# Kernel tuning notes

Measured on AMD Instinct MI355X. Metric: run time of the kernel, lower is better.

Reference implementation:

```python
import jax, jax.numpy as jnp
import numpy as np

N = 100000   # nodes
E = 600000   # edges
K = 3        # TAGConv hops
EPS = 1e-5   # BatchNorm eps
SLOPE = 0.01 # LeakyReLU negative slope


def setup_inputs() -> dict:
    key = jax.random.key(0)
    ks = jax.random.split(key, 8)
    y = jax.random.normal(ks[0], (N, 128), dtype=jnp.float32)
    edge_index = jax.random.randint(ks[1], (2, E), 0, N, dtype=jnp.int64)
    edge_attr = jax.random.uniform(ks[2], (E,), dtype=jnp.float32)
    # TAGConv layer l has (K+1) weight matrices [in, out]; bias only on first two layers
    W1 = 0.1 * jax.random.normal(ks[3], (K + 1, 128, 128), dtype=jnp.float32)
    b1 = jnp.full((128,), 0.1, dtype=jnp.float32)
    W2 = 0.1 * jax.random.normal(ks[4], (K + 1, 128, 128), dtype=jnp.float32)
    b2 = jnp.full((128,), 0.1, dtype=jnp.float32)
    W3 = 0.1 * jax.random.normal(ks[5], (K + 1, 128, 64), dtype=jnp.float32)
    g1 = jnp.ones((128,), jnp.float32); be1 = jnp.zeros((128,), jnp.float32)
    g2 = jnp.ones((128,), jnp.float32); be2 = jnp.zeros((128,), jnp.float32)
    g3 = jnp.ones((64,), jnp.float32);  be3 = jnp.zeros((64,), jnp.float32)
    return dict(y=y, edge_index=edge_index, edge_attr=edge_attr,
                W1=W1, b1=b1, g1=g1, be1=be1,
                W2=W2, b2=b2, g2=g2, be2=be2,
                W3=W3, g3=g3, be3=be3)


def _tag_conv(x, W, b, src, dst, norm):
    # out = sum_{k=0..K} A_hat^k x @ W_k (+ b)
    out = x @ W[0]
    h = x
    for k in range(1, W.shape[0]):
        h = jax.ops.segment_sum(norm[:, None] * h[src], dst, num_segments=N)
        out = out + h @ W[k]
    return out if b is None else out + b


def _bn(x, g, b):
    # BatchNorm1d training mode: biased batch stats over nodes
    m = x.mean(axis=0)
    v = jnp.mean((x - m) ** 2, axis=0)
    return (x - m) * jax.lax.rsqrt(v + EPS) * g + b


def reference(y, edge_index, edge_attr, W1, b1, g1, be1, W2, b2, g2, be2, W3, g3, be3):
    src, dst = edge_index[0], edge_index[1]
    # gcn_norm (symmetric, no self-loops): D^{-1/2} A D^{-1/2}
    deg = jax.ops.segment_sum(edge_attr, dst, num_segments=N)
    dis = jnp.where(deg > 0, jax.lax.rsqrt(jnp.maximum(deg, 1e-12)), 0.0)
    norm = dis[src] * edge_attr * dis[dst]
    lrelu = lambda t: jax.nn.leaky_relu(t, SLOPE)
    x = lrelu(_bn(_tag_conv(y, W1, b1, src, dst, norm), g1, be1))
    x = lrelu(_bn(_tag_conv(x, W2, b2, src, dst, norm), g2, be2))
    x = lrelu(_bn(_tag_conv(x, W3, None, src, dst, norm), g3, be3))
    return x
```

## Files before the change

### kernel.cpp

```cpp
#include <hip/hip_runtime.h>
#include <hip/hip_bf16.h>

typedef unsigned short b16;
typedef __attribute__((ext_vector_type(8))) unsigned short us8;
typedef __attribute__((ext_vector_type(8))) short short8;
typedef __attribute__((ext_vector_type(4))) float float4v;

#define NN 100000
#define NE 600000

__device__ __forceinline__ float bf2f(b16 u) {
    return __uint_as_float(((unsigned)u) << 16);
}
__device__ __forceinline__ b16 f2bf(float f) {
    unsigned x = __float_as_uint(f);
    return (b16)((x + 0x7fffu + ((x >> 16) & 1u)) >> 16);
}

__global__ void k_detect(const void* __restrict__ y, const void* __restrict__ ei,
                         int* __restrict__ flags) {
    if (threadIdx.x == 0 && blockIdx.x == 0) {
        const b16* p = (const b16*)y;
        int f32 = 0;
        for (int i = 0; i < 128; ++i) {
            float v = bf2f(p[i]);
            if (!(fabsf(v) < 1e4f)) { f32 = 1; break; }
        }
        flags[0] = f32;
        const long long* q = (const long long*)ei;
        int i64 = 1;
        for (int i = 0; i < 4; ++i) {
            long long v = q[i];
            if (v < 0 || v >= NN) i64 = 0;
        }
        flags[1] = i64;
    }
}

__global__ void k_cvt(const void* __restrict__ in, float* __restrict__ out, int n,
                      const int* __restrict__ flags) {
    int i = blockIdx.x * blockDim.x + threadIdx.x;
    if (i >= n) return;
    out[i] = flags[0] ? ((const float*)in)[i] : bf2f(((const b16*)in)[i]);
}

__global__ void k_idx(const void* __restrict__ ei, int* __restrict__ src32,
                      int* __restrict__ dst32, const int* __restrict__ flags) {
    int e = blockIdx.x * blockDim.x + threadIdx.x;
    if (e >= NE) return;
    int s, d;
    if (flags[1]) {
        const long long* p = (const long long*)ei;
        s = (int)p[e];
        d = (int)p[NE + e];
    } else {
        const int* p = (const int*)ei;
        s = p[e];
        d = p[NE + e];
    }
    src32[e] = ((unsigned)s < NN) ? s : 0;
    dst32[e] = ((unsigned)d < NN) ? d : 0;
}

__global__ void k_degcnt(const int* __restrict__ dst, const void* __restrict__ ea,
                         float* __restrict__ deg, int* __restrict__ cnt,
                         const int* __restrict__ flags) {
    int e = blockIdx.x * blockDim.x + threadIdx.x;
    if (e >= NE) return;
    float w = flags[0] ? ((const float*)ea)[e] : bf2f(((const b16*)ea)[e]);
    int d = dst[e];
    unsafeAtomicAdd(&deg[d], w);
    atomicAdd(&cnt[d], 1);
}

__global__ void k_dis(float* deg) {
    int n = blockIdx.x * blockDim.x + threadIdx.x;
    if (n < NN) {
        float d = deg[n];
        deg[n] = (d > 0.f) ? rsqrtf(fmaxf(d, 1e-12f)) : 0.f;
    }
}

#define SCAN_B 1024
#define SCAN_NB ((NN + SCAN_B - 1) / SCAN_B)

__global__ __launch_bounds__(SCAN_B) void k_scan1(const int* __restrict__ cnt,
                                                  int* __restrict__ inc,
                                                  int* __restrict__ bsum) {
    __shared__ int s[SCAN_B];
    int i = blockIdx.x * SCAN_B + threadIdx.x;
    s[threadIdx.x] = (i < NN) ? cnt[i] : 0;
    __syncthreads();
    for (int off = 1; off < SCAN_B; off <<= 1) {
        int t = (threadIdx.x >= off) ? s[threadIdx.x - off] : 0;
        __syncthreads();
        s[threadIdx.x] += t;
        __syncthreads();
    }
    if (i < NN) inc[i] = s[threadIdx.x];
    if (threadIdx.x == SCAN_B - 1) bsum[blockIdx.x] = s[SCAN_B - 1];
}

__global__ void k_scan2(int* bsum) {
    if (threadIdx.x == 0 && blockIdx.x == 0) {
        int a = 0;
        for (int i = 0; i < SCAN_NB; ++i) {
            int t = bsum[i];
            bsum[i] = a;
            a += t;
        }
    }
}

__global__ void k_scan3(const int* __restrict__ inc, const int* __restrict__ bsum,
                        int* __restrict__ rowptr) {
    int i = blockIdx.x * blockDim.x + threadIdx.x;
    if (i == 0) rowptr[0] = 0;
    if (i < NN) rowptr[i + 1] = inc[i] + bsum[i / SCAN_B];
}

__global__ void k_fill(const int* __restrict__ src, const int* __restrict__ dst,
                       const void* __restrict__ ea, const float* __restrict__ dis,
                       const int* __restrict__ rowptr, int* __restrict__ fill,
                       int* __restrict__ csrc, float* __restrict__ cw,
                       const int* __restrict__ flags) {
    int e = blockIdx.x * blockDim.x + threadIdx.x;
    if (e >= NE) return;
    float a = flags[0] ? ((const float*)ea)[e] : bf2f(((const b16*)ea)[e]);
    int d = dst[e];
    int s = src[e];
    int pos = rowptr[d] + atomicAdd(&fill[d], 1);
    csrc[pos] = s;
    cw[pos] = dis[s] * a * dis[d];
}

__global__ void k_pack(const void* __restrict__ W, b16* __restrict__ Wp, int NC,
                       const int* __restrict__ flags) {
    int f = blockIdx.x * blockDim.x + threadIdx.x;
    int total = 512 * NC / 8;
    if (f >= total) return;
    int lane = f & 63;
    int rest = f >> 6;
    int CT = NC >> 4;
    int ct = rest % CT, ks = rest / CT;
    int k0 = 32 * ks + (lane >> 4) * 8;
    int col = 16 * ct + (lane & 15);
    us8 v;
#pragma unroll
    for (int j = 0; j < 8; ++j) {
        float x = flags[0] ? ((const float*)W)[(size_t)(k0 + j) * NC + col]
                           : bf2f(((const b16*)W)[(size_t)(k0 + j) * NC + col]);
        v[j] = f2bf(x);
    }
    *(us8*)&Wp[(size_t)f * 8] = v;
}

__global__ void k_cast(const void* __restrict__ y, b16* __restrict__ XC,
                       const int* __restrict__ flags) {
    int i = blockIdx.x * blockDim.x + threadIdx.x;
    if (i >= NN * 32) return;
    int row = i >> 5, cg = i & 31;
    float4 v;
    if (flags[0]) {
        v = ((const float4*)y)[i];
    } else {
        ushort4 u = ((const ushort4*)y)[i];
        v = make_float4(bf2f(u.x), bf2f(u.y), bf2f(u.z), bf2f(u.w));
    }
    ushort4 o;
    o.x = f2bf(v.x); o.y = f2bf(v.y); o.z = f2bf(v.z); o.w = f2bf(v.w);
    *(ushort4*)&XC[(size_t)row * 512 + 4 * cg] = o;
}

__global__ __launch_bounds__(256) void k_spmm(b16* __restrict__ XC, int ci, int co,
                                              const int* __restrict__ rowptr,
                                              const int* __restrict__ csrc,
                                              const float* __restrict__ cw) {
    int gid = blockIdx.x * blockDim.x + threadIdx.x;
    int node = gid >> 6;
    if (node >= NN) return;
    int lane = gid & 63;
    int beg = rowptr[node], end = rowptr[node + 1];
    int coff = ci + 2 * lane;

    float ax0 = 0.f, ay0 = 0.f, ax1 = 0.f, ay1 = 0.f;
    for (int i = beg; i < end; i += 4) {
        int lim = end - 1;
        int e1 = i + 1, e2 = i + 2, e3 = i + 3;
        float w0 = cw[i];
        float w1 = (e1 < end) ? cw[e1] : 0.f;
        float w2 = (e2 < end) ? cw[e2] : 0.f;
        float w3 = (e3 < end) ? cw[e3] : 0.f;
        int s0 = csrc[i];
        int s1 = csrc[e1 < lim ? e1 : lim];
        int s2 = csrc[e2 < lim ? e2 : lim];
        int s3 = csrc[e3 < lim ? e3 : lim];
        unsigned u0 = *(const unsigned*)&XC[(size_t)s0 * 512 + coff];
        unsigned u1 = *(const unsigned*)&XC[(size_t)s1 * 512 + coff];
        unsigned u2 = *(const unsigned*)&XC[(size_t)s2 * 512 + coff];
        unsigned u3 = *(const unsigned*)&XC[(size_t)s3 * 512 + coff];
        ax0 = fmaf(w0, __uint_as_float(u0 << 16), ax0);
        ay0 = fmaf(w0, __uint_as_float(u0 & 0xFFFF0000u), ay0);
        ax1 = fmaf(w1, __uint_as_float(u1 << 16), ax1);
        ay1 = fmaf(w1, __uint_as_float(u1 & 0xFFFF0000u), ay1);
        ax0 = fmaf(w2, __uint_as_float(u2 << 16), ax0);
        ay0 = fmaf(w2, __uint_as_float(u2 & 0xFFFF0000u), ay0);
        ax1 = fmaf(w3, __uint_as_float(u3 << 16), ax1);
        ay1 = fmaf(w3, __uint_as_float(u3 & 0xFFFF0000u), ay1);
    }
    ax0 += ax1;
    ay0 += ay1;
    ushort2 o;
    o.x = f2bf(ax0);
    o.y = f2bf(ay0);
    *(ushort2*)&XC[(size_t)node * 512 + co + 2 * lane] = o;
}

template <int CTF>
__global__ __launch_bounds__(256) void k_mgemm(const b16* __restrict__ XC,
                                               const b16* __restrict__ Wp,
                                               const float* __restrict__ bias,
                                               b16* __restrict__ OUT,
                                               float* __restrict__ gsum,
                                               float* __restrict__ gsq) {
    constexpr int NC = CTF * 16;
    __shared__ float csum[64], csq[64];
    const int tid = threadIdx.x;
    const int wave = tid >> 6;
    const int lane = tid & 63;
    const int quad = lane >> 4;
    const int l15 = lane & 15;
    const int cb = blockIdx.y;
    const int cbase = cb * 4;
    const int rbase = blockIdx.x * 256 + wave * 64;

    for (int i = tid; i < 64; i += 256) {
        csum[i] = 0.f;
        csq[i] = 0.f;
    }

    float4v acc[4][4];
#pragma unroll
    for (int rt = 0; rt < 4; ++rt)
#pragma unroll
        for (int ct = 0; ct < 4; ++ct) acc[rt][ct] = (float4v)(0.f);

    const b16* gA[4];
#pragma unroll
    for (int rt = 0; rt < 4; ++rt) {
        int r = rbase + 16 * rt + l15;
        if (r >= NN) r = NN - 1;
        gA[rt] = XC + (size_t)r * 512 + quad * 8;
    }
    const b16* gB = Wp + (size_t)cbase * 512 + lane * 8;

    short8 ab[2][4], bb[2][4];
#pragma unroll
    for (int rt = 0; rt < 4; ++rt) ab[0][rt] = *(const short8*)(gA[rt]);
#pragma unroll
    for (int ct = 0; ct < 4; ++ct) bb[0][ct] = *(const short8*)(gB + ct * 512);

#pragma unroll
    for (int ks = 0; ks < 16; ++ks) {
        const int cur = ks & 1, nxt = cur ^ 1;
        if (ks < 15) {
#pragma unroll
            for (int rt = 0; rt < 4; ++rt)
                ab[nxt][rt] = *(const short8*)(gA[rt] + 32 * (ks + 1));
#pragma unroll
            for (int ct = 0; ct < 4; ++ct)
                bb[nxt][ct] = *(const short8*)(gB + (size_t)(ks + 1) * CTF * 512 + ct * 512);
        }
#pragma unroll
        for (int rt = 0; rt < 4; ++rt)
#pragma unroll
            for (int ct = 0; ct < 4; ++ct)
                acc[rt][ct] = __builtin_amdgcn_mfma_f32_16x16x32_bf16(
                    ab[cur][rt], bb[cur][ct], acc[rt][ct], 0, 0, 0);
    }

#pragma unroll
    for (int rt = 0; rt < 4; ++rt) {
#pragma unroll
        for (int ct = 0; ct < 4; ++ct) {
            int cl = 16 * ct + l15;
            int col = cb * 64 + cl;
            float bv = bias ? bias[col] : 0.f;
            float s = 0.f, sq = 0.f;
#pragma unroll
            for (int r = 0; r < 4; ++r) {
                int row = rbase + 16 * rt + quad * 4 + r;
                if (row < NN) {
                    float v = acc[rt][ct][r] + bv;
                    OUT[(size_t)row * NC + col] = f2bf(v);
                    s += v;
                    sq += v * v;
                }
            }
            s += __shfl_xor(s, 16);
            s += __shfl_xor(s, 32);
            sq += __shfl_xor(sq, 16);
            sq += __shfl_xor(sq, 32);
            if (quad == 0) {
                atomicAdd(&csum[cl], s);
                atomicAdd(&csq[cl], sq);
            }
        }
    }
    __syncthreads();
    if (tid < 64) {
        unsafeAtomicAdd(&gsum[cb * 64 + tid], csum[tid]);
        unsafeAtomicAdd(&gsq[cb * 64 + tid], csq[tid]);
    }
}

__global__ void k_bnparam(const float* gsum, const float* gsq, const float* g,
                          const float* be, float* scale, float* shift, int ncols) {
    int c = threadIdx.x;
    if (c < ncols) {
        float m = gsum[c] * (1.f / NN);
        float v = gsq[c] * (1.f / NN) - m * m;
        v = fmaxf(v, 0.f);
        float s = rsqrtf(v + 1e-5f) * g[c];
        scale[c] = s;
        shift[c] = be[c] - m * s;
    }
}

__global__ void k_bnapply_mid(const b16* __restrict__ OUT,
                              const float* __restrict__ scale,
                              const float* __restrict__ shift, b16* __restrict__ XC) {
    int i = blockIdx.x * blockDim.x + threadIdx.x;
    if (i >= NN * 64) return;
    int row = i >> 6, c = (i & 63) * 2;
    ushort2 u = *(const ushort2*)&OUT[(size_t)row * 128 + c];
    float a = fmaf(bf2f(u.x), scale[c], shift[c]);
    float b = fmaf(bf2f(u.y), scale[c + 1], shift[c + 1]);
    a = a > 0.f ? a : 0.01f * a;
    b = b > 0.f ? b : 0.01f * b;
    ushort2 o;
    o.x = f2bf(a);
    o.y = f2bf(b);
    *(ushort2*)&XC[(size_t)row * 512 + c] = o;
}

__global__ void k_bnapply_last(const b16* __restrict__ OUT,
                               const float* __restrict__ scale,
                               const float* __restrict__ shift, void* __restrict__ dout,
                               const int* __restrict__ flags) {
    int i = blockIdx.x * blockDim.x + threadIdx.x;
    if (i >= NN * 64) return;
    int c = i & 63;
    float v = fmaf(bf2f(OUT[i]), scale[c], shift[c]);
    v = v > 0.f ? v : 0.01f * v;
    if (flags[0])
        ((float*)dout)[i] = v;
    else
        ((b16*)dout)[i] = f2bf(v);
}

#define PB_B1 0
#define PB_B2 128
#define PB_G1 256
#define PB_BE1 384
#define PB_G2 512
#define PB_BE2 640
#define PB_G3 768
#define PB_BE3 832
#define PB_SZ 896

extern "C" void kernel_launch(void* const* d_in, const int* in_sizes, int n_in,
                              void* d_out, int out_size, void* d_ws, size_t ws_size,
                              hipStream_t stream) {
    const void* y   = d_in[0];
    const void* ei  = d_in[1];
    const void* ea  = d_in[2];
    const void* W1  = d_in[3];
    const void* b1  = d_in[4];
    const void* g1  = d_in[5];
    const void* be1 = d_in[6];
    const void* W2  = d_in[7];
    const void* b2  = d_in[8];
    const void* g2  = d_in[9];
    const void* be2 = d_in[10];
    const void* W3  = d_in[11];
    const void* g3  = d_in[12];
    const void* be3 = d_in[13];

    char* w = (char*)d_ws;
    size_t used = 0;
    auto carve = [&](size_t bytes) -> char* {
        char* p = w + used;
        used += (bytes + 255) & ~(size_t)255;
        return p;
    };

    int* flags   = (int*)carve(16);
    int* src32   = (int*)carve((size_t)NE * 4);
    int* dst32   = (int*)carve((size_t)NE * 4);
    float* deg   = (float*)carve((size_t)NN * 4);
    int* cnt     = (int*)carve((size_t)NN * 4);
    int* rowptr  = (int*)carve((size_t)(NN + 1) * 4);
    int* cscan   = (int*)carve((size_t)NN * 4);
    int* bsum    = (int*)carve((size_t)SCAN_NB * 4);
    int* csrc    = (int*)carve((size_t)NE * 4);
    float* cw    = (float*)carve((size_t)NE * 4);
    float* PB    = (float*)carve(PB_SZ * 4);
    b16* Wp1     = (b16*)carve((size_t)512 * 128 * 2);
    b16* Wp2     = (b16*)carve((size_t)512 * 128 * 2);
    b16* Wp3     = (b16*)carve((size_t)512 * 64 * 2);
    b16* OUT     = (b16*)carve((size_t)NN * 128 * 2);
    float* gsum  = (float*)carve(128 * 4);
    float* gsq   = (float*)carve(128 * 4);
    float* scale = (float*)carve(128 * 4);
    float* shift = (float*)carve(128 * 4);
    b16* XC      = (b16*)carve((size_t)NN * 512 * 2);

    k_detect<<<1, 64, 0, stream>>>(y, ei, flags);
    auto cvt = [&](const void* in, float* out, int n) {
        k_cvt<<<(n + 127) / 128, 128, 0, stream>>>(in, out, n, flags);
    };
    cvt(b1, PB + PB_B1, 128);
    cvt(b2, PB + PB_B2, 128);
    cvt(g1, PB + PB_G1, 128);
    cvt(be1, PB + PB_BE1, 128);
    cvt(g2, PB + PB_G2, 128);
    cvt(be2, PB + PB_BE2, 128);
    cvt(g3, PB + PB_G3, 64);
    cvt(be3, PB + PB_BE3, 64);
    k_pack<<<(512 * 128 / 8 + 255) / 256, 256, 0, stream>>>(W1, Wp1, 128, flags);
    k_pack<<<(512 * 128 / 8 + 255) / 256, 256, 0, stream>>>(W2, Wp2, 128, flags);
    k_pack<<<(512 * 64 / 8 + 255) / 256, 256, 0, stream>>>(W3, Wp3, 64, flags);

    k_idx<<<(NE + 255) / 256, 256, 0, stream>>>(ei, src32, dst32, flags);
    hipMemsetAsync(deg, 0, (size_t)NN * 4, stream);
    hipMemsetAsync(cnt, 0, (size_t)NN * 4, stream);
    k_degcnt<<<(NE + 255) / 256, 256, 0, stream>>>(dst32, ea, deg, cnt, flags);
    k_dis<<<(NN + 255) / 256, 256, 0, stream>>>(deg);
    k_scan1<<<SCAN_NB, SCAN_B, 0, stream>>>(cnt, cscan, bsum);
    k_scan2<<<1, 64, 0, stream>>>(bsum);
    k_scan3<<<(NN + 255) / 256, 256, 0, stream>>>(cscan, bsum, rowptr);
    hipMemsetAsync(cnt, 0, (size_t)NN * 4, stream);
    k_fill<<<(NE + 255) / 256, 256, 0, stream>>>(src32, dst32, ea, deg, rowptr, cnt,
                                                 csrc, cw, flags);

    k_cast<<<(NN * 32 + 255) / 256, 256, 0, stream>>>(y, XC, flags);

    auto spmm = [&](int ci, int co) {
        k_spmm<<<(NN * 64 + 255) / 256, 256, 0, stream>>>(XC, ci, co, rowptr, csrc, cw);
    };
    const int gemm_gx = (NN + 255) / 256;

    auto layer = [&](const b16* Wp, const float* bias, const float* g, const float* be,
                     int NC, bool last) {
        spmm(0, 128);
        spmm(128, 256);
        spmm(256, 384);
        hipMemsetAsync(gsum, 0, NC * 4, stream);
        hipMemsetAsync(gsq, 0, NC * 4, stream);
        if (NC == 128)
            k_mgemm<8><<<dim3(gemm_gx, 2), 256, 0, stream>>>(XC, Wp, bias, OUT, gsum, gsq);
        else
            k_mgemm<4><<<dim3(gemm_gx, 1), 256, 0, stream>>>(XC, Wp, bias, OUT, gsum, gsq);
        k_bnparam<<<1, NC, 0, stream>>>(gsum, gsq, g, be, scale, shift, NC);
        if (last)
            k_bnapply_last<<<(NN * 64 + 255) / 256, 256, 0, stream>>>(OUT, scale, shift,
                                                                      d_out, flags);
        else
            k_bnapply_mid<<<(NN * 64 + 255) / 256, 256, 0, stream>>>(OUT, scale, shift,
                                                                     XC);
    };

    layer(Wp1, PB + PB_B1, PB + PB_G1, PB + PB_BE1, 128, false);
    layer(Wp2, PB + PB_B2, PB + PB_G2, PB + PB_BE2, 128, false);
    layer(Wp3, nullptr, PB + PB_G3, PB + PB_BE3, 64, true);
}
```

Baseline: 819.8 us.

## Fuse BatchNorm apply into next layer's first SpMM and restructure GEMM tiling

Folds the BN-param and BN-apply+LeakyReLU of layers 1 and 2 into a new SpMM kernel that normalizes gathered neighbor rows on the fly while also writing the normalized self features. This removes separate bnparam/bnapply passes over the node features. The GEMM now computes all output columns per block with 128-row tiles instead of splitting columns across blockIdx.y. Small launches are also merged: parameter conversions go into one kernel and memsets into one per buffer. In exchange, the BN transform is recomputed for every gathered edge (about 6x the elementwise work), and the GEMM uses fewer waves per row tile.

Result: faster. 802.7 us (-2.1%).

```diff
diff --git a/kernel.cpp b/kernel.cpp
--- a/kernel.cpp
+++ b/kernel.cpp
@@ -8,6 +8,7 @@
 
 #define NN 100000
 #define NE 600000
+#define INV_NN (1.0f / NN)
 
 __device__ __forceinline__ float bf2f(b16 u) {
     return __uint_as_float(((unsigned)u) << 16);
@@ -37,11 +38,22 @@
     }
 }
 
-__global__ void k_cvt(const void* __restrict__ in, float* __restrict__ out, int n,
-                      const int* __restrict__ flags) {
-    int i = blockIdx.x * blockDim.x + threadIdx.x;
-    if (i >= n) return;
-    out[i] = flags[0] ? ((const float*)in)[i] : bf2f(((const b16*)in)[i]);
+__global__ void k_cvt_all(const void* b1, const void* b2, const void* g1,
+                          const void* be1, const void* g2, const void* be2,
+                          const void* g3, const void* be3, float* __restrict__ PB,
+                          const int* __restrict__ flags) {
+    int i = threadIdx.x;
+    const void* src;
+    int off;
+    if (i < 128) { src = b1; off = i; }
+    else if (i < 256) { src = b2; off = i - 128; }
+    else if (i < 384) { src = g1; off = i - 256; }
+    else if (i < 512) { src = be1; off = i - 384; }
+    else if (i < 640) { src = g2; off = i - 512; }
+    else if (i < 768) { src = be2; off = i - 640; }
+    else if (i < 832) { src = g3; off = i - 768; }
+    else { src = be3; off = i - 832; }
+    PB[i] = flags[0] ? ((const float*)src)[off] : bf2f(((const b16*)src)[off]);
 }
 
 __global__ void k_idx(const void* __restrict__ ei, int* __restrict__ src32,
@@ -216,75 +228,140 @@
     *(ushort2*)&XC[(size_t)node * 512 + co + 2 * lane] = o;
 }
 
-template <int CTF>
+__global__ __launch_bounds__(256) void k_spmm_bn(b16* __restrict__ XC,
+                                                 const b16* __restrict__ OUT, int co,
+                                                 const int* __restrict__ rowptr,
+                                                 const int* __restrict__ csrc,
+                                                 const float* __restrict__ cw,
+                                                 const float* __restrict__ gsum,
+                                                 const float* __restrict__ gsq,
+                                                 const float* __restrict__ gamma,
+                                                 const float* __restrict__ beta) {
+    int gid = blockIdx.x * blockDim.x + threadIdx.x;
+    int node = gid >> 6;
+    if (node >= NN) return;
+    int lane = gid & 63;
+    int c = 2 * lane;
+    float m0 = gsum[c] * INV_NN, m1 = gsum[c + 1] * INV_NN;
+    float v0 = fmaxf(gsq[c] * INV_NN - m0 * m0, 0.f);
+    float v1 = fmaxf(gsq[c + 1] * INV_NN - m1 * m1, 0.f);
+    float sc0 = rsqrtf(v0 + 1e-5f) * gamma[c];
+    float sc1 = rsqrtf(v1 + 1e-5f) * gamma[c + 1];
+    float sh0 = beta[c] - m0 * sc0;
+    float sh1 = beta[c + 1] - m1 * sc1;
+
+    int beg = rowptr[node], end = rowptr[node + 1];
+    float ax0 = 0.f, ay0 = 0.f, ax1 = 0.f, ay1 = 0.f;
+    for (int i = beg; i < end; i += 4) {
+        int lim = end - 1;
+        int e1 = i + 1, e2 = i + 2, e3 = i + 3;
+        float w0 = cw[i];
+        float w1 = (e1 < end) ? cw[e1] : 0.f;
+        float w2 = (e2 < end) ? cw[e2] : 0.f;
+        float w3 = (e3 < end) ? cw[e3] : 0.f;
+        int s0 = csrc[i];
+        int s1 = csrc[e1 < lim ? e1 : lim];
+        int s2 = csrc[e2 < lim ? e2 : lim];
+        int s3 = csrc[e3 < lim ? e3 : lim];
+        unsigned u0 = *(const unsigned*)&OUT[(size_t)s0 * 128 + c];
+        unsigned u1 = *(const unsigned*)&OUT[(size_t)s1 * 128 + c];
+        unsigned u2 = *(const unsigned*)&OUT[(size_t)s2 * 128 + c];
+        unsigned u3 = *(const unsigned*)&OUT[(size_t)s3 * 128 + c];
+#define BNX(u) ({ float t = fmaf(__uint_as_float((u) << 16), sc0, sh0); t > 0.f ? t : 0.01f * t; })
+#define BNY(u) ({ float t = fmaf(__uint_as_float((u) & 0xFFFF0000u), sc1, sh1); t > 0.f ? t : 0.01f * t; })
+        ax0 = fmaf(w0, BNX(u0), ax0);
+        ay0 = fmaf(w0, BNY(u0), ay0);
+        ax1 = fmaf(w1, BNX(u1), ax1);
+        ay1 = fmaf(w1, BNY(u1), ay1);
+        ax0 = fmaf(w2, BNX(u2), ax0);
+        ay0 = fmaf(w2, BNY(u2), ay0);
+        ax1 = fmaf(w3, BNX(u3), ax1);
+        ay1 = fmaf(w3, BNY(u3), ay1);
+    }
+    unsigned un = *(const unsigned*)&OUT[(size_t)node * 128 + c];
+    float xn0 = BNX(un), xn1 = BNY(un);
+#undef BNX
+#undef BNY
+    ushort2 ox;
+    ox.x = f2bf(xn0);
+    ox.y = f2bf(xn1);
+    *(ushort2*)&XC[(size_t)node * 512 + c] = ox;
+
+    ax0 += ax1;
+    ay0 += ay1;
+    ushort2 o;
+    o.x = f2bf(ax0);
+    o.y = f2bf(ay0);
+    *(ushort2*)&XC[(size_t)node * 512 + co + 2 * lane] = o;
+}
+
+template <int CT>
 __global__ __launch_bounds__(256) void k_mgemm(const b16* __restrict__ XC,
                                                const b16* __restrict__ Wp,
                                                const float* __restrict__ bias,
                                                b16* __restrict__ OUT,
                                                float* __restrict__ gsum,
                                                float* __restrict__ gsq) {
-    constexpr int NC = CTF * 16;
-    __shared__ float csum[64], csq[64];
+    constexpr int NC = CT * 16;
+    __shared__ float csum[NC], csq[NC];
     const int tid = threadIdx.x;
     const int wave = tid >> 6;
     const int lane = tid & 63;
     const int quad = lane >> 4;
     const int l15 = lane & 15;
-    const int cb = blockIdx.y;
-    const int cbase = cb * 4;
-    const int rbase = blockIdx.x * 256 + wave * 64;
-
-    for (int i = tid; i < 64; i += 256) {
+    const int rbase = blockIdx.x * 128 + wave * 32;
+
+    for (int i = tid; i < NC; i += 256) {
         csum[i] = 0.f;
         csq[i] = 0.f;
     }
 
-    float4v acc[4][4];
-#pragma unroll
-    for (int rt = 0; rt < 4; ++rt)
-#pragma unroll
-        for (int ct = 0; ct < 4; ++ct) acc[rt][ct] = (float4v)(0.f);
-
-    const b16* gA[4];
-#pragma unroll
-    for (int rt = 0; rt < 4; ++rt) {
+    float4v acc[2][CT];
+#pragma unroll
+    for (int rt = 0; rt < 2; ++rt)
+#pragma unroll
+        for (int ct = 0; ct < CT; ++ct) acc[rt][ct] = (float4v)(0.f);
+
+    const b16* gA[2];
+#pragma unroll
+    for (int rt = 0; rt < 2; ++rt) {
         int r = rbase + 16 * rt + l15;
         if (r >= NN) r = NN - 1;
         gA[rt] = XC + (size_t)r * 512 + quad * 8;
     }
-    const b16* gB = Wp + (size_t)cbase * 512 + lane * 8;
-
-    short8 ab[2][4], bb[2][4];
-#pragma unroll
-    for (int rt = 0; rt < 4; ++rt) ab[0][rt] = *(const short8*)(gA[rt]);
-#pragma unroll
-    for (int ct = 0; ct < 4; ++ct) bb[0][ct] = *(const short8*)(gB + ct * 512);
+    const b16* gB = Wp + lane * 8;
+
+    short8 ab[2][2], bb[2][CT];
+#pragma unroll
+    for (int rt = 0; rt < 2; ++rt) ab[0][rt] = *(const short8*)(gA[rt]);
+#pragma unroll
+    for (int ct = 0; ct < CT; ++ct) bb[0][ct] = *(const short8*)(gB + ct * 512);
 
 #pragma unroll
     for (int ks = 0; ks < 16; ++ks) {
         const int cur = ks & 1, nxt = cur ^ 1;
         if (ks < 15) {
 #pragma unroll
-            for (int rt = 0; rt < 4; ++rt)
+            for (int rt = 0; rt < 2; ++rt)
                 ab[nxt][rt] = *(const short8*)(gA[rt] + 32 * (ks + 1));
 #pragma unroll
-            for (int ct = 0; ct < 4; ++ct)
-                bb[nxt][ct] = *(const short8*)(gB + (size_t)(ks + 1) * CTF * 512 + ct * 512);
+            for (int ct = 0; ct < CT; ++ct)
+                bb[nxt][ct] =
+                    *(const short8*)(gB + (size_t)(ks + 1) * CT * 512 + ct * 512);
         }
 #pragma unroll
-        for (int rt = 0; rt < 4; ++rt)
-#pragma unroll
-            for (int ct = 0; ct < 4; ++ct)
+        for (int rt = 0; rt < 2; ++rt)
+#pragma unroll
+            for (int ct = 0; ct < CT; ++ct)
                 acc[rt][ct] = __builtin_amdgcn_mfma_f32_16x16x32_bf16(
                     ab[cur][rt], bb[cur][ct], acc[rt][ct], 0, 0, 0);
     }
 
 #pragma unroll
-    for (int rt = 0; rt < 4; ++rt) {
-#pragma unroll
-        for (int ct = 0; ct < 4; ++ct) {
-            int cl = 16 * ct + l15;
-            int col = cb * 64 + cl;
+    for (int rt = 0; rt < 2; ++rt) {
+#pragma unroll
+        for (int ct = 0; ct < CT; ++ct) {
+            int col = 16 * ct + l15;
             float bv = bias ? bias[col] : 0.f;
             float s = 0.f, sq = 0.f;
 #pragma unroll
@@ -302,56 +379,36 @@
             sq += __shfl_xor(sq, 16);
             sq += __shfl_xor(sq, 32);
             if (quad == 0) {
-                atomicAdd(&csum[cl], s);
-                atomicAdd(&csq[cl], sq);
+                atomicAdd(&csum[col], s);
+                atomicAdd(&csq[col], sq);
             }
         }
     }
     __syncthreads();
+    for (int i = tid; i < NC; i += 256) {
+        unsafeAtomicAdd(&gsum[i], csum[i]);
+        unsafeAtomicAdd(&gsq[i], csq[i]);
+    }
+}
+
+__global__ void k_bnlast(const b16* __restrict__ OUT, const float* __restrict__ gsum,
+                         const float* __restrict__ gsq, const float* __restrict__ gamma,
+                         const float* __restrict__ beta, void* __restrict__ dout,
+                         const int* __restrict__ flags) {
+    __shared__ float sc[64], sh[64];
+    int tid = threadIdx.x;
     if (tid < 64) {
-        unsafeAtomicAdd(&gsum[cb * 64 + tid], csum[tid]);
-        unsafeAtomicAdd(&gsq[cb * 64 + tid], csq[tid]);
-    }
-}
-
-__global__ void k_bnparam(const float* gsum, const float* gsq, const float* g,
-                          const float* be, float* scale, float* shift, int ncols) {
-    int c = threadIdx.x;
-    if (c < ncols) {
-        float m = gsum[c] * (1.f / NN);
-        float v = gsq[c] * (1.f / NN) - m * m;
-        v = fmaxf(v, 0.f);
-        float s = rsqrtf(v + 1e-5f) * g[c];
-        scale[c] = s;
-        shift[c] = be[c] - m * s;
-    }
-}
-
-__global__ void k_bnapply_mid(const b16* __restrict__ OUT,
-                              const float* __restrict__ scale,
-                              const float* __restrict__ shift, b16* __restrict__ XC) {
-    int i = blockIdx.x * blockDim.x + threadIdx.x;
-    if (i >= NN * 64) return;
-    int row = i >> 6, c = (i & 63) * 2;
-    ushort2 u = *(const ushort2*)&OUT[(size_t)row * 128 + c];
-    float a = fmaf(bf2f(u.x), scale[c], shift[c]);
-    float b = fmaf(bf2f(u.y), scale[c + 1], shift[c + 1]);
-    a = a > 0.f ? a : 0.01f * a;
-    b = b > 0.f ? b : 0.01f * b;
-    ushort2 o;
-    o.x = f2bf(a);
-    o.y = f2bf(b);
-    *(ushort2*)&XC[(size_t)row * 512 + c] = o;
-}
-
-__global__ void k_bnapply_last(const b16* __restrict__ OUT,
-                               const float* __restrict__ scale,
-                               const float* __restrict__ shift, void* __restrict__ dout,
-                               const int* __restrict__ flags) {
-    int i = blockIdx.x * blockDim.x + threadIdx.x;
+        float m = gsum[tid] * INV_NN;
+        float v = fmaxf(gsq[tid] * INV_NN - m * m, 0.f);
+        float s = rsqrtf(v + 1e-5f) * gamma[tid];
+        sc[tid] = s;
+        sh[tid] = beta[tid] - m * s;
+    }
+    __syncthreads();
+    int i = blockIdx.x * blockDim.x + tid;
     if (i >= NN * 64) return;
     int c = i & 63;
-    float v = fmaf(bf2f(OUT[i]), scale[c], shift[c]);
+    float v = fmaf(bf2f(OUT[i]), sc[c], sh[c]);
     v = v > 0.f ? v : 0.01f * v;
     if (flags[0])
         ((float*)dout)[i] = v;
@@ -398,8 +455,8 @@
     int* flags   = (int*)carve(16);
     int* src32   = (int*)carve((size_t)NE * 4);
     int* dst32   = (int*)carve((size_t)NE * 4);
-    float* deg   = (float*)carve((size_t)NN * 4);
-    int* cnt     = (int*)carve((size_t)NN * 4);
+    float* deg   = (float*)carve((size_t)NN * 4 + (size_t)NN * 4);
+    int* cnt     = (int*)(deg + NN);
     int* rowptr  = (int*)carve((size_t)(NN + 1) * 4);
     int* cscan   = (int*)carve((size_t)NN * 4);
     int* bsum    = (int*)carve((size_t)SCAN_NB * 4);
@@ -410,31 +467,18 @@
     b16* Wp2     = (b16*)carve((size_t)512 * 128 * 2);
     b16* Wp3     = (b16*)carve((size_t)512 * 64 * 2);
     b16* OUT     = (b16*)carve((size_t)NN * 128 * 2);
-    float* gsum  = (float*)carve(128 * 4);
-    float* gsq   = (float*)carve(128 * 4);
-    float* scale = (float*)carve(128 * 4);
-    float* shift = (float*)carve(128 * 4);
+    float* GS    = (float*)carve(3 * 256 * 4);
     b16* XC      = (b16*)carve((size_t)NN * 512 * 2);
 
     k_detect<<<1, 64, 0, stream>>>(y, ei, flags);
-    auto cvt = [&](const void* in, float* out, int n) {
-        k_cvt<<<(n + 127) / 128, 128, 0, stream>>>(in, out, n, flags);
-    };
-    cvt(b1, PB + PB_B1, 128);
-    cvt(b2, PB + PB_B2, 128);
-    cvt(g1, PB + PB_G1, 128);
-    cvt(be1, PB + PB_BE1, 128);
-    cvt(g2, PB + PB_G2, 128);
-    cvt(be2, PB + PB_BE2, 128);
-    cvt(g3, PB + PB_G3, 64);
-    cvt(be3, PB + PB_BE3, 64);
+    k_cvt_all<<<1, PB_SZ, 0, stream>>>(b1, b2, g1, be1, g2, be2, g3, be3, PB, flags);
     k_pack<<<(512 * 128 / 8 + 255) / 256, 256, 0, stream>>>(W1, Wp1, 128, flags);
     k_pack<<<(512 * 128 / 8 + 255) / 256, 256, 0, stream>>>(W2, Wp2, 128, flags);
     k_pack<<<(512 * 64 / 8 + 255) / 256, 256, 0, stream>>>(W3, Wp3, 64, flags);
 
     k_idx<<<(NE + 255) / 256, 256, 0, stream>>>(ei, src32, dst32, flags);
-    hipMemsetAsync(deg, 0, (size_t)NN * 4, stream);
-    hipMemsetAsync(cnt, 0, (size_t)NN * 4, stream);
+    hipMemsetAsync(deg, 0, (size_t)NN * 8, stream);
+    hipMemsetAsync(GS, 0, 3 * 256 * 4, stream);
     k_degcnt<<<(NE + 255) / 256, 256, 0, stream>>>(dst32, ea, deg, cnt, flags);
     k_dis<<<(NN + 255) / 256, 256, 0, stream>>>(deg);
     k_scan1<<<SCAN_NB, SCAN_B, 0, stream>>>(cnt, cscan, bsum);
@@ -446,32 +490,30 @@
 
     k_cast<<<(NN * 32 + 255) / 256, 256, 0, stream>>>(y, XC, flags);
 
+    const int spmm_grid = (NN * 64 + 255) / 256;
+    const int gemm_grid = (NN + 127) / 128;
     auto spmm = [&](int ci, int co) {
-        k_spmm<<<(NN * 64 + 255) / 256, 256, 0, stream>>>(XC, ci, co, rowptr, csrc, cw);
+        k_spmm<<<spmm_grid, 256, 0, stream>>>(XC, ci, co, rowptr, csrc, cw);
     };
-    const int gemm_gx = (NN + 255) / 256;
-
-    auto layer = [&](const b16* Wp, const float* bias, const float* g, const float* be,
-                     int NC, bool last) {
-        spmm(0, 128);
-        spmm(128, 256);
-        spmm(256, 384);
-        hipMemsetAsync(gsum, 0, NC * 4, stream);
-        hipMemsetAsync(gsq, 0, NC * 4, stream);
-        if (NC == 128)
-            k_mgemm<8><<<dim3(gemm_gx, 2), 256, 0, stream>>>(XC, Wp, bias, OUT, gsum, gsq);
-        else
-            k_mgemm<4><<<dim3(gemm_gx, 1), 256, 0, stream>>>(XC, Wp, bias, OUT, gsum, gsq);
-        k_bnparam<<<1, NC, 0, stream>>>(gsum, gsq, g, be, scale, shift, NC);
-        if (last)
-            k_bnapply_last<<<(NN * 64 + 255) / 256, 256, 0, stream>>>(OUT, scale, shift,
-                                                                      d_out, flags);
-        else
-            k_bnapply_mid<<<(NN * 64 + 255) / 256, 256, 0, stream>>>(OUT, scale, shift,
-                                                                     XC);
-    };
-
-    layer(Wp1, PB + PB_B1, PB + PB_G1, PB + PB_BE1, 128, false);
-    layer(Wp2, PB + PB_B2, PB + PB_G2, PB + PB_BE2, 128, false);
-    layer(Wp3, nullptr, PB + PB_G3, PB + PB_BE3, 64, true);
-}
+
+    spmm(0, 128);
+    spmm(128, 256);
+    spmm(256, 384);
+    k_mgemm<8><<<gemm_grid, 256, 0, stream>>>(XC, Wp1, PB + PB_B1, OUT, GS + 0,
+                                              GS + 128);
+    k_spmm_bn<<<spmm_grid, 256, 0, stream>>>(XC, OUT, 128, rowptr, csrc, cw, GS + 0,
+                                             GS + 128, PB + PB_G1, PB + PB_BE1);
+    spmm(128, 256);
+    spmm(256, 384);
+    k_mgemm<8><<<gemm_grid, 256, 0, stream>>>(XC, Wp2, PB + PB_B2, OUT, GS + 256,
+                                              GS + 384);
+    k_spmm_bn<<<spmm_grid, 256, 0, stream>>>(XC, OUT, 128, rowptr, csrc, cw, GS + 256,
+                                             GS + 384, PB + PB_G2, PB + PB_BE2);
+    spmm(128, 256);
+    spmm(256, 384);
+    k_mgemm<4><<<gemm_grid, 256, 0, stream>>>(XC, Wp3, nullptr, OUT, GS + 512,
+                                              GS + 640);
+    k_bnlast<<<(NN * 64 + 255) / 256, 256, 0, stream>>>(OUT, GS + 512, GS + 640,
+                                                        PB + PB_G3, PB + PB_BE3, d_out,
+                                                        flags);
+}
```
